# Kernel tuning notes

Measured on AMD Instinct MI355X. Metric: run time of the kernel, lower is better.

## Reference

```python
import jax, jax.numpy as jnp
import numpy as np

B, P, H, D = 32, 512, 512, 512

def setup_inputs() -> dict:
    key = jax.random.key(0)
    k1, k2, k3, k4 = jax.random.split(key, 4)
    px = jax.random.normal(k1, (B, P, D), dtype=jnp.float32)
    hx = jax.random.normal(k2, (B, H, D), dtype=jnp.float32)
    p_mask = jax.random.randint(k3, (B, P), 0, 2) == 1  # True = padded
    h_mask = jax.random.randint(k4, (B, H), 0, 2) == 1
    return {"px": px, "hx": hx, "p_mask": p_mask, "h_mask": h_mask}

def reference(px, hx, p_mask, h_mask):
    # shared (unscaled) score matrix: [B, P, H]
    e = jnp.einsum('bpd,bhd->bph', px, hx)
    neg_inf = jnp.float32(-jnp.inf)
    h_bias = jnp.where(h_mask, neg_inf, 0.0).astype(e.dtype)  # [B, H]
    p_bias = jnp.where(p_mask, neg_inf, 0.0).astype(e.dtype)  # [B, P]
    # softmax over hypothesis axis -> attend px to hx
    weight_b = jax.nn.softmax(e + h_bias[:, None, :], axis=2)  # [B, P, H]
    px_hat = jnp.einsum('bph,bhd->bpd', weight_b, hx)
    # softmax over premise axis -> attend hx to px
    weight_a = jax.nn.softmax(e + p_bias[:, :, None], axis=1)  # [B, P, H]
    hx_hat = jnp.einsum('bph,bpd->bhd', weight_a, px)
    m_p = jnp.concatenate([px, px_hat, px - px_hat, px * px_hat], axis=-1)
    m_h = jnp.concatenate([hx, hx_hat, hx - hx_hat, hx * hx_hat], axis=-1)
    return (m_p, m_h)
```

## Files before the change

kernel.cpp:

```cpp
#include <hip/hip_runtime.h>
#include <math.h>

#define NB 32
#define NN 512
#define ROWC 2048ull

typedef __attribute__((ext_vector_type(8))) short bf16x8;
typedef __attribute__((ext_vector_type(4))) float f32x4;

__device__ __forceinline__ unsigned int fbits(float f) {
  union { float f; unsigned int u; } v; v.f = f; return v.u;
}
__device__ __forceinline__ float bcast(unsigned int u) {
  union { unsigned int u; float f; } v; v.u = u; return v.f;
}
__device__ __forceinline__ unsigned int bf16_rne(float f) {
  unsigned int b = fbits(f);
  return (b + 0x7FFFu + ((b >> 16) & 1u)) >> 16;
}

__device__ __forceinline__ float wave_red_max(float v) {
#pragma unroll
  for (int o = 32; o > 0; o >>= 1) v = fmaxf(v, __shfl_down(v, o));
  return v;
}
__device__ __forceinline__ float wave_red_sum(float v) {
#pragma unroll
  for (int o = 32; o > 0; o >>= 1) v += __shfl_down(v, o);
  return v;
}

__device__ __forceinline__ int frag_byte(int blk, int lane, int khalf) {
  int base = ((((khalf << 3) + blk) << 6) + lane) << 4;
  int swz = (blk ^ (lane >> 4) ^ (khalf << 2)) & 7;
  return base ^ (swz << 4);
}

__device__ __forceinline__ void stage_hilo(const float* __restrict__ src, int row0, int k0,
                                           char* __restrict__ Lh, char* __restrict__ Ll,
                                           int t) {
#pragma unroll
  for (int i = 0; i < 8; ++i) {
    int idx = i * 256 + t;
    int r = idx >> 4, c4 = idx & 15;
    int k = c4 << 2;
    float4 f = *(const float4*)&src[(size_t)(row0 + r) * NN + k0 + k];
    unsigned int b0 = fbits(f.x), b1 = fbits(f.y), b2 = fbits(f.z), b3 = fbits(f.w);
    unsigned int h01 = (b0 >> 16) | (b1 & 0xFFFF0000u);
    unsigned int h23 = (b2 >> 16) | (b3 & 0xFFFF0000u);
    float r0 = f.x - bcast(b0 & 0xFFFF0000u);
    float r1 = f.y - bcast(b1 & 0xFFFF0000u);
    float r2 = f.z - bcast(b2 & 0xFFFF0000u);
    float r3 = f.w - bcast(b3 & 0xFFFF0000u);
    unsigned int l01 = (fbits(r0) >> 16) | (fbits(r1) & 0xFFFF0000u);
    unsigned int l23 = (fbits(r2) >> 16) | (fbits(r3) & 0xFFFF0000u);
    int khalf = k >> 5, k8 = (k >> 3) & 3, j = k & 7;
    int byte = frag_byte(r >> 4, (r & 15) + (k8 << 4), khalf) + (j << 1);
    *(uint2*)(Lh + byte) = make_uint2(h01, h23);
    *(uint2*)(Ll + byte) = make_uint2(l01, l23);
  }
}

__global__ __launch_bounds__(256) void gemm_e(const float* __restrict__ px,
                                              const float* __restrict__ hx,
                                              float* __restrict__ e) {
  __shared__ char Ah[16384], Al[16384], Bh[16384], Bl[16384];
  const int b = blockIdx.z;
  const float* A = px + (size_t)b * NN * NN;
  const float* B = hx + (size_t)b * NN * NN;
  float* C = e + (size_t)b * NN * NN;
  const int row0 = blockIdx.y * 128, col0 = blockIdx.x * 128;
  const int t = threadIdx.x;
  const int l = t & 63, w = t >> 6;
  const int wr = w >> 1, wc = w & 1;

  f32x4 acc[4][4];
#pragma unroll
  for (int i = 0; i < 4; ++i)
#pragma unroll
    for (int j = 0; j < 4; ++j)
#pragma unroll
      for (int r = 0; r < 4; ++r) acc[i][j][r] = 0.f;

  for (int k0 = 0; k0 < NN; k0 += 64) {
    stage_hilo(A, row0, k0, Ah, Al, t);
    stage_hilo(B, col0, k0, Bh, Bl, t);
    __syncthreads();
#pragma unroll
    for (int kh = 0; kh < 2; ++kh) {
      bf16x8 ah[4], al[4], bh[4], bl[4];
#pragma unroll
      for (int i = 0; i < 4; ++i) {
        int ab = frag_byte(wr * 4 + i, l, kh);
        ah[i] = *(const bf16x8*)(Ah + ab);
        al[i] = *(const bf16x8*)(Al + ab);
        int bb = frag_byte(wc * 4 + i, l, kh);
        bh[i] = *(const bf16x8*)(Bh + bb);
        bl[i] = *(const bf16x8*)(Bl + bb);
      }
#pragma unroll
      for (int i = 0; i < 4; ++i)
#pragma unroll
        for (int j = 0; j < 4; ++j) {
          acc[i][j] = __builtin_amdgcn_mfma_f32_16x16x32_bf16(ah[i], bh[j], acc[i][j], 0, 0, 0);
          acc[i][j] = __builtin_amdgcn_mfma_f32_16x16x32_bf16(ah[i], bl[j], acc[i][j], 0, 0, 0);
          acc[i][j] = __builtin_amdgcn_mfma_f32_16x16x32_bf16(al[i], bh[j], acc[i][j], 0, 0, 0);
        }
    }
    __syncthreads();
  }
  const int g = l >> 4, li = l & 15;
#pragma unroll
  for (int i = 0; i < 4; ++i)
#pragma unroll
    for (int j = 0; j < 4; ++j)
#pragma unroll
      for (int r = 0; r < 4; ++r) {
        int row = row0 + wr * 64 + i * 16 + g * 4 + r;
        int col = col0 + wc * 64 + j * 16 + li;
        C[(size_t)row * NN + col] = acc[i][j][r];
      }
}

__global__ __launch_bounds__(256) void softmax_h(const float* __restrict__ e,
                                                 const int* __restrict__ h_mask,
                                                 unsigned short* __restrict__ wb) {
  const int bp = blockIdx.x;
  const int b = bp >> 9;
  const float* row = e + (size_t)bp * NN;
  unsigned short* outp = wb + (size_t)bp * NN;
  const int* hm = h_mask + (size_t)b * NN;
  const int t = threadIdx.x;
  float2 v = *(const float2*)&row[2 * t];
  int2 m = *(const int2*)&hm[2 * t];
  float v0 = m.x ? -INFINITY : v.x;
  float v1 = m.y ? -INFINITY : v.y;
  __shared__ float pm[4], ps[4];
  float mx = wave_red_max(fmaxf(v0, v1));
  if ((t & 63) == 0) pm[t >> 6] = mx;
  __syncthreads();
  mx = fmaxf(fmaxf(pm[0], pm[1]), fmaxf(pm[2], pm[3]));
  float e0 = __expf(v0 - mx), e1 = __expf(v1 - mx);
  float s = wave_red_sum(e0 + e1);
  if ((t & 63) == 0) ps[t >> 6] = s;
  __syncthreads();
  s = ps[0] + ps[1] + ps[2] + ps[3];
  float inv = 1.0f / s;
  unsigned int u0 = bf16_rne(e0 * inv), u1 = bf16_rne(e1 * inv);
  *(unsigned int*)&outp[2 * t] = u0 | (u1 << 16);
}

__global__ __launch_bounds__(256) void softmax_p(const float* __restrict__ e,
                                                 const int* __restrict__ p_mask,
                                                 unsigned short* __restrict__ waT) {
  const int b = blockIdx.y;
  const int h0 = blockIdx.x * 32;
  const int t = threadIdx.x;
  const int tx = t & 31, ty = t >> 5;
  const float* eb = e + (size_t)b * NN * NN;
  const int* pmask = p_mask + (size_t)b * NN;
  const int h = h0 + tx;
  float val[64];
  float mx = -INFINITY;
#pragma unroll
  for (int k = 0; k < 64; ++k) {
    int p = ty + (k << 3);
    float v = pmask[p] ? -INFINITY : eb[(size_t)p * NN + h];
    val[k] = v;
    mx = fmaxf(mx, v);
  }
  __shared__ float rm[8][33];
  __shared__ unsigned short tile[32][516];
  rm[ty][tx] = mx;
  __syncthreads();
  float gm = rm[0][tx];
#pragma unroll
  for (int rr = 1; rr < 8; ++rr) gm = fmaxf(gm, rm[rr][tx]);
  float s = 0.f;
#pragma unroll
  for (int k = 0; k < 64; ++k) {
    val[k] = __expf(val[k] - gm);
    s += val[k];
  }
  __syncthreads();
  rm[ty][tx] = s;
  __syncthreads();
  float gs = rm[0][tx];
#pragma unroll
  for (int rr = 1; rr < 8; ++rr) gs += rm[rr][tx];
  float inv = 1.0f / gs;
#pragma unroll
  for (int k = 0; k < 64; ++k) {
    int p = ty + (k << 3);
    tile[tx][p] = (unsigned short)bf16_rne(val[k] * inv);
  }
  __syncthreads();
  unsigned short* wt = waT + ((size_t)b * NN + h0) * NN;
#pragma unroll
  for (int i = 0; i < 16; ++i) {
    int idx = i * 256 + t;
    int r = idx >> 7, c4 = idx & 127;
    *(uint2*)&wt[(size_t)r * NN + c4 * 4] = *(const uint2*)&tile[r][c4 * 4];
  }
}

__global__ __launch_bounds__(256) void gemm_wv(const unsigned short* __restrict__ Wg,
                                               const float* __restrict__ Bsrc,
                                               const float* __restrict__ Xg,
                                               float* __restrict__ outg) {
  __shared__ union {
    struct { char A[16384]; char B[16384]; } s;
    float ep[64][132];
  } u;
  const int b = blockIdx.z;
  const unsigned short* A = Wg + (size_t)b * NN * NN;
  const float* B = Bsrc + (size_t)b * NN * NN;
  const float* X = Xg + (size_t)b * NN * NN;
  float* out = outg + (size_t)b * NN * ROWC;
  const int row0 = blockIdx.y * 128, col0 = blockIdx.x * 128;
  const int t = threadIdx.x;
  const int l = t & 63, w = t >> 6;
  const int wr = w >> 1, wc = w & 1;

  f32x4 acc[4][4];
#pragma unroll
  for (int i = 0; i < 4; ++i)
#pragma unroll
    for (int j = 0; j < 4; ++j)
#pragma unroll
      for (int r = 0; r < 4; ++r) acc[i][j][r] = 0.f;

  for (int k0 = 0; k0 < NN; k0 += 64) {
#pragma unroll
    for (int i = 0; i < 8; ++i) {
      int idx = i * 256 + t;
      int r = idx >> 4, c4 = idx & 15, k = c4 << 2;
      uint2 v = *(const uint2*)&A[(size_t)(row0 + r) * NN + k0 + k];
      int khalf = k >> 5, k8 = (k >> 3) & 3, j = k & 7;
      int byte = frag_byte(r >> 4, (r & 15) + (k8 << 4), khalf) + (j << 1);
      *(uint2*)(u.s.A + byte) = v;
    }
#pragma unroll
    for (int i = 0; i < 4; ++i) {
      int idx = i * 256 + t;
      int kp = idx >> 5, nq = idx & 31;
      int k = kp << 1, n = nq << 2;
      const float* p0 = &B[(size_t)(k0 + k) * NN + col0 + n];
      float4 f0 = *(const float4*)p0;
      float4 f1 = *(const float4*)(p0 + NN);
      int khalf = k >> 5, k8 = (k >> 3) & 3, j = k & 7;
      float fa0[4] = {f0.x, f0.y, f0.z, f0.w};
      float fa1[4] = {f1.x, f1.y, f1.z, f1.w};
#pragma unroll
      for (int c = 0; c < 4; ++c) {
        unsigned int pk = bf16_rne(fa0[c]) | (bf16_rne(fa1[c]) << 16);
        int nn2 = n + c;
        int byte = frag_byte(nn2 >> 4, (nn2 & 15) + (k8 << 4), khalf) + (j << 1);
        *(unsigned int*)(u.s.B + byte) = pk;
      }
    }
    __syncthreads();
#pragma unroll
    for (int kh = 0; kh < 2; ++kh) {
      bf16x8 av[4], bv[4];
#pragma unroll
      for (int i = 0; i < 4; ++i) {
        av[i] = *(const bf16x8*)(u.s.A + frag_byte(wr * 4 + i, l, kh));
        bv[i] = *(const bf16x8*)(u.s.B + frag_byte(wc * 4 + i, l, kh));
      }
#pragma unroll
      for (int i = 0; i < 4; ++i)
#pragma unroll
        for (int j = 0; j < 4; ++j)
          acc[i][j] = __builtin_amdgcn_mfma_f32_16x16x32_bf16(av[i], bv[j], acc[i][j], 0, 0, 0);
    }
    __syncthreads();
  }

  const int g = l >> 4, li = l & 15;
#pragma unroll
  for (int pass = 0; pass < 2; ++pass) {
    if (wr == pass) {
#pragma unroll
      for (int i = 0; i < 4; ++i)
#pragma unroll
        for (int j = 0; j < 4; ++j)
#pragma unroll
          for (int r = 0; r < 4; ++r)
            u.ep[i * 16 + g * 4 + r][wc * 64 + j * 16 + li] = acc[i][j][r];
    }
    __syncthreads();
#pragma unroll
    for (int i = 0; i < 8; ++i) {
      int idx = i * 256 + t;
      int r = idx >> 5, c4 = idx & 31;
      int grow = row0 + pass * 64 + r;
      float4 ph = *(const float4*)&u.ep[r][c4 * 4];
      float4 xv = *(const float4*)&X[(size_t)grow * NN + col0 + c4 * 4];
      size_t base = (size_t)grow * ROWC + col0 + c4 * 4;
      *(float4*)&out[base] = xv;
      *(float4*)&out[base + 512] = ph;
      float4 df = {xv.x - ph.x, xv.y - ph.y, xv.z - ph.z, xv.w - ph.w};
      *(float4*)&out[base + 1024] = df;
      float4 pr = {xv.x * ph.x, xv.y * ph.y, xv.z * ph.z, xv.w * ph.w};
      *(float4*)&out[base + 1536] = pr;
    }
    __syncthreads();
  }
}

extern "C" void kernel_launch(void* const* d_in, const int* in_sizes, int n_in,
                              void* d_out, int out_size, void* d_ws, size_t ws_size,
                              hipStream_t stream) {
  const float* px = (const float*)d_in[0];
  const float* hx = (const float*)d_in[1];
  const int* p_mask = (const int*)d_in[2];
  const int* h_mask = (const int*)d_in[3];
  float* out = (float*)d_out;

  float* e = (float*)d_ws;
  unsigned short* wb = (unsigned short*)(e + (size_t)NB * NN * NN);
  unsigned short* waT = wb + (size_t)NB * NN * NN;

  dim3 blk(256);
  dim3 gg(4, 4, NB);
  gemm_e<<<gg, blk, 0, stream>>>(px, hx, e);
  softmax_h<<<dim3(NB * NN), blk, 0, stream>>>(e, h_mask, wb);
  softmax_p<<<dim3(16, NB), blk, 0, stream>>>(e, p_mask, waT);
  gemm_wv<<<gg, blk, 0, stream>>>(wb, hx, px, out);
  gemm_wv<<<gg, blk, 0, stream>>>(waT, px, hx, out + (size_t)NB * NN * ROWC);
}
```

Before: 242.6 us.

## Fuse softmax statistics into score GEMM epilogue and recompute weights in consumer GEMMs

Result: faster. 214.8 us (-11.5%).

```diff
diff --git a/kernel.cpp b/kernel.cpp
--- a/kernel.cpp
+++ b/kernel.cpp
@@ -17,17 +17,6 @@
 __device__ __forceinline__ unsigned int bf16_rne(float f) {
   unsigned int b = fbits(f);
   return (b + 0x7FFFu + ((b >> 16) & 1u)) >> 16;
-}
-
-__device__ __forceinline__ float wave_red_max(float v) {
-#pragma unroll
-  for (int o = 32; o > 0; o >>= 1) v = fmaxf(v, __shfl_down(v, o));
-  return v;
-}
-__device__ __forceinline__ float wave_red_sum(float v) {
-#pragma unroll
-  for (int o = 32; o > 0; o >>= 1) v += __shfl_down(v, o);
-  return v;
 }
 
 __device__ __forceinline__ int frag_byte(int blk, int lane, int khalf) {
@@ -61,10 +50,15 @@
   }
 }
 
-__global__ __launch_bounds__(256) void gemm_e(const float* __restrict__ px,
-                                              const float* __restrict__ hx,
-                                              float* __restrict__ e) {
+__global__ __launch_bounds__(256) void gemm_e_stats(
+    const float* __restrict__ px, const float* __restrict__ hx,
+    const int* __restrict__ p_mask, const int* __restrict__ h_mask,
+    float* __restrict__ e,
+    float* __restrict__ rpm, float* __restrict__ rps,
+    float* __restrict__ cpm, float* __restrict__ cps) {
   __shared__ char Ah[16384], Al[16384], Bh[16384], Bl[16384];
+  __shared__ int pmk[128], hmk[128];
+  __shared__ float st_m[2][128], st_s[2][128], sc_m[2][128], sc_s[2][128];
   const int b = blockIdx.z;
   const float* A = px + (size_t)b * NN * NN;
   const float* B = hx + (size_t)b * NN * NN;
@@ -73,6 +67,10 @@
   const int t = threadIdx.x;
   const int l = t & 63, w = t >> 6;
   const int wr = w >> 1, wc = w & 1;
+  const int g = l >> 4, li = l & 15;
+
+  if (t < 128) pmk[t] = p_mask[(size_t)b * NN + row0 + t];
+  else hmk[t - 128] = h_mask[(size_t)b * NN + col0 + (t - 128)];
 
   f32x4 acc[4][4];
 #pragma unroll
@@ -109,7 +107,7 @@
     }
     __syncthreads();
   }
-  const int g = l >> 4, li = l & 15;
+
 #pragma unroll
   for (int i = 0; i < 4; ++i)
 #pragma unroll
@@ -120,108 +118,132 @@
         int col = col0 + wc * 64 + j * 16 + li;
         C[(size_t)row * NN + col] = acc[i][j][r];
       }
-}
-
-__global__ __launch_bounds__(256) void softmax_h(const float* __restrict__ e,
-                                                 const int* __restrict__ h_mask,
-                                                 unsigned short* __restrict__ wb) {
-  const int bp = blockIdx.x;
-  const int b = bp >> 9;
-  const float* row = e + (size_t)bp * NN;
-  unsigned short* outp = wb + (size_t)bp * NN;
-  const int* hm = h_mask + (size_t)b * NN;
+
+#pragma unroll
+  for (int i = 0; i < 4; ++i)
+#pragma unroll
+    for (int r = 0; r < 4; ++r) {
+      float v[4];
+      float m = -INFINITY;
+#pragma unroll
+      for (int j = 0; j < 4; ++j) {
+        v[j] = hmk[wc * 64 + j * 16 + li] ? -INFINITY : acc[i][j][r];
+        m = fmaxf(m, v[j]);
+      }
+#pragma unroll
+      for (int o = 1; o < 16; o <<= 1) m = fmaxf(m, __shfl_xor(m, o));
+      float s = 0.f;
+#pragma unroll
+      for (int j = 0; j < 4; ++j) s += (v[j] == -INFINITY) ? 0.f : __expf(v[j] - m);
+#pragma unroll
+      for (int o = 1; o < 16; o <<= 1) s += __shfl_xor(s, o);
+      if (li == 0) {
+        st_m[wc][wr * 64 + i * 16 + g * 4 + r] = m;
+        st_s[wc][wr * 64 + i * 16 + g * 4 + r] = s;
+      }
+    }
+
+#pragma unroll
+  for (int j = 0; j < 4; ++j) {
+    float v[16];
+    float m = -INFINITY;
+#pragma unroll
+    for (int i = 0; i < 4; ++i)
+#pragma unroll
+      for (int r = 0; r < 4; ++r) {
+        float x = pmk[wr * 64 + i * 16 + g * 4 + r] ? -INFINITY : acc[i][j][r];
+        v[i * 4 + r] = x;
+        m = fmaxf(m, x);
+      }
+    m = fmaxf(m, __shfl_xor(m, 16));
+    m = fmaxf(m, __shfl_xor(m, 32));
+    float s = 0.f;
+#pragma unroll
+    for (int q = 0; q < 16; ++q) s += (v[q] == -INFINITY) ? 0.f : __expf(v[q] - m);
+    s += __shfl_xor(s, 16);
+    s += __shfl_xor(s, 32);
+    if (g == 0) {
+      sc_m[wr][wc * 64 + j * 16 + li] = m;
+      sc_s[wr][wc * 64 + j * 16 + li] = s;
+    }
+  }
+  __syncthreads();
+
+  if (t < 128) {
+    float m0 = st_m[0][t], m1 = st_m[1][t];
+    float s0 = st_s[0][t], s1 = st_s[1][t];
+    float m = fmaxf(m0, m1);
+    float s = 0.f;
+    if (s0 > 0.f) s += s0 * __expf(m0 - m);
+    if (s1 > 0.f) s += s1 * __expf(m1 - m);
+    rpm[((size_t)b * 4 + blockIdx.x) * NN + row0 + t] = m;
+    rps[((size_t)b * 4 + blockIdx.x) * NN + row0 + t] = s;
+  } else {
+    int c = t - 128;
+    float m0 = sc_m[0][c], m1 = sc_m[1][c];
+    float s0 = sc_s[0][c], s1 = sc_s[1][c];
+    float m = fmaxf(m0, m1);
+    float s = 0.f;
+    if (s0 > 0.f) s += s0 * __expf(m0 - m);
+    if (s1 > 0.f) s += s1 * __expf(m1 - m);
+    cpm[((size_t)b * 4 + blockIdx.y) * NN + col0 + c] = m;
+    cps[((size_t)b * 4 + blockIdx.y) * NN + col0 + c] = s;
+  }
+}
+
+__global__ __launch_bounds__(512) void merge_stats(
+    const float* __restrict__ rpm, const float* __restrict__ rps,
+    const float* __restrict__ cpm, const float* __restrict__ cps,
+    float* __restrict__ rmax, float* __restrict__ rinv,
+    float* __restrict__ cmax, float* __restrict__ cinv) {
+  const int b = blockIdx.x;
   const int t = threadIdx.x;
-  float2 v = *(const float2*)&row[2 * t];
-  int2 m = *(const int2*)&hm[2 * t];
-  float v0 = m.x ? -INFINITY : v.x;
-  float v1 = m.y ? -INFINITY : v.y;
-  __shared__ float pm[4], ps[4];
-  float mx = wave_red_max(fmaxf(v0, v1));
-  if ((t & 63) == 0) pm[t >> 6] = mx;
-  __syncthreads();
-  mx = fmaxf(fmaxf(pm[0], pm[1]), fmaxf(pm[2], pm[3]));
-  float e0 = __expf(v0 - mx), e1 = __expf(v1 - mx);
-  float s = wave_red_sum(e0 + e1);
-  if ((t & 63) == 0) ps[t >> 6] = s;
-  __syncthreads();
-  s = ps[0] + ps[1] + ps[2] + ps[3];
-  float inv = 1.0f / s;
-  unsigned int u0 = bf16_rne(e0 * inv), u1 = bf16_rne(e1 * inv);
-  *(unsigned int*)&outp[2 * t] = u0 | (u1 << 16);
-}
-
-__global__ __launch_bounds__(256) void softmax_p(const float* __restrict__ e,
-                                                 const int* __restrict__ p_mask,
-                                                 unsigned short* __restrict__ waT) {
-  const int b = blockIdx.y;
-  const int h0 = blockIdx.x * 32;
-  const int t = threadIdx.x;
-  const int tx = t & 31, ty = t >> 5;
-  const float* eb = e + (size_t)b * NN * NN;
-  const int* pmask = p_mask + (size_t)b * NN;
-  const int h = h0 + tx;
-  float val[64];
-  float mx = -INFINITY;
-#pragma unroll
-  for (int k = 0; k < 64; ++k) {
-    int p = ty + (k << 3);
-    float v = pmask[p] ? -INFINITY : eb[(size_t)p * NN + h];
-    val[k] = v;
-    mx = fmaxf(mx, v);
-  }
-  __shared__ float rm[8][33];
-  __shared__ unsigned short tile[32][516];
-  rm[ty][tx] = mx;
-  __syncthreads();
-  float gm = rm[0][tx];
-#pragma unroll
-  for (int rr = 1; rr < 8; ++rr) gm = fmaxf(gm, rm[rr][tx]);
+  const float* pm = blockIdx.y == 0 ? rpm : cpm;
+  const float* ps = blockIdx.y == 0 ? rps : cps;
+  float* fm = blockIdx.y == 0 ? rmax : cmax;
+  float* fi = blockIdx.y == 0 ? rinv : cinv;
+  float mj[4], sj[4];
+  float m = -INFINITY;
+#pragma unroll
+  for (int j = 0; j < 4; ++j) {
+    mj[j] = pm[((size_t)b * 4 + j) * NN + t];
+    sj[j] = ps[((size_t)b * 4 + j) * NN + t];
+    m = fmaxf(m, mj[j]);
+  }
   float s = 0.f;
 #pragma unroll
-  for (int k = 0; k < 64; ++k) {
-    val[k] = __expf(val[k] - gm);
-    s += val[k];
-  }
-  __syncthreads();
-  rm[ty][tx] = s;
-  __syncthreads();
-  float gs = rm[0][tx];
-#pragma unroll
-  for (int rr = 1; rr < 8; ++rr) gs += rm[rr][tx];
-  float inv = 1.0f / gs;
-#pragma unroll
-  for (int k = 0; k < 64; ++k) {
-    int p = ty + (k << 3);
-    tile[tx][p] = (unsigned short)bf16_rne(val[k] * inv);
-  }
-  __syncthreads();
-  unsigned short* wt = waT + ((size_t)b * NN + h0) * NN;
-#pragma unroll
-  for (int i = 0; i < 16; ++i) {
-    int idx = i * 256 + t;
-    int r = idx >> 7, c4 = idx & 127;
-    *(uint2*)&wt[(size_t)r * NN + c4 * 4] = *(const uint2*)&tile[r][c4 * 4];
-  }
-}
-
-__global__ __launch_bounds__(256) void gemm_wv(const unsigned short* __restrict__ Wg,
-                                               const float* __restrict__ Bsrc,
-                                               const float* __restrict__ Xg,
-                                               float* __restrict__ outg) {
+  for (int j = 0; j < 4; ++j)
+    if (sj[j] > 0.f) s += sj[j] * __expf(mj[j] - m);
+  fm[(size_t)b * NN + t] = m;
+  fi[(size_t)b * NN + t] = 1.0f / s;
+}
+
+__global__ __launch_bounds__(256) void gemm_wp(
+    const float* __restrict__ E, const float* __restrict__ hxg,
+    const float* __restrict__ pxg, const int* __restrict__ h_mask,
+    const float* __restrict__ rmax, const float* __restrict__ rinv,
+    float* __restrict__ outg) {
   __shared__ union {
     struct { char A[16384]; char B[16384]; } s;
     float ep[64][132];
   } u;
   const int b = blockIdx.z;
-  const unsigned short* A = Wg + (size_t)b * NN * NN;
-  const float* B = Bsrc + (size_t)b * NN * NN;
-  const float* X = Xg + (size_t)b * NN * NN;
+  const float* Eb = E + (size_t)b * NN * NN;
+  const float* B = hxg + (size_t)b * NN * NN;
+  const float* X = pxg + (size_t)b * NN * NN;
+  const int* hm = h_mask + (size_t)b * NN;
+  const float* rmx = rmax + (size_t)b * NN;
+  const float* rin = rinv + (size_t)b * NN;
   float* out = outg + (size_t)b * NN * ROWC;
   const int row0 = blockIdx.y * 128, col0 = blockIdx.x * 128;
   const int t = threadIdx.x;
   const int l = t & 63, w = t >> 6;
   const int wr = w >> 1, wc = w & 1;
 
+  float rmv[8];
+#pragma unroll
+  for (int i = 0; i < 8; ++i) rmv[i] = rmx[row0 + ((i * 256 + t) >> 4)];
+
   f32x4 acc[4][4];
 #pragma unroll
   for (int i = 0; i < 4; ++i)
@@ -235,10 +257,17 @@
     for (int i = 0; i < 8; ++i) {
       int idx = i * 256 + t;
       int r = idx >> 4, c4 = idx & 15, k = c4 << 2;
-      uint2 v = *(const uint2*)&A[(size_t)(row0 + r) * NN + k0 + k];
+      float4 f = *(const float4*)&Eb[(size_t)(row0 + r) * NN + k0 + k];
+      int4 m4 = *(const int4*)&hm[k0 + k];
+      float w0 = m4.x ? 0.f : __expf(f.x - rmv[i]);
+      float w1 = m4.y ? 0.f : __expf(f.y - rmv[i]);
+      float w2 = m4.z ? 0.f : __expf(f.z - rmv[i]);
+      float w3 = m4.w ? 0.f : __expf(f.w - rmv[i]);
+      unsigned int p01 = bf16_rne(w0) | (bf16_rne(w1) << 16);
+      unsigned int p23 = bf16_rne(w2) | (bf16_rne(w3) << 16);
       int khalf = k >> 5, k8 = (k >> 3) & 3, j = k & 7;
       int byte = frag_byte(r >> 4, (r & 15) + (k8 << 4), khalf) + (j << 1);
-      *(uint2*)(u.s.A + byte) = v;
+      *(uint2*)(u.s.A + byte) = make_uint2(p01, p23);
     }
 #pragma unroll
     for (int i = 0; i < 4; ++i) {
@@ -295,7 +324,9 @@
       int idx = i * 256 + t;
       int r = idx >> 5, c4 = idx & 31;
       int grow = row0 + pass * 64 + r;
+      float ri = rin[grow];
       float4 ph = *(const float4*)&u.ep[r][c4 * 4];
+      ph.x *= ri; ph.y *= ri; ph.z *= ri; ph.w *= ri;
       float4 xv = *(const float4*)&X[(size_t)grow * NN + col0 + c4 * 4];
       size_t base = (size_t)grow * ROWC + col0 + c4 * 4;
       *(float4*)&out[base] = xv;
@@ -309,6 +340,139 @@
   }
 }
 
+__global__ __launch_bounds__(256) void gemm_wh(
+    const float* __restrict__ E, const float* __restrict__ pxg,
+    const float* __restrict__ hxg, const int* __restrict__ p_mask,
+    const float* __restrict__ cmax, const float* __restrict__ cinv,
+    float* __restrict__ outg) {
+  __shared__ union {
+    struct { char A[16384]; char B[16384]; } s;
+    float ep[64][132];
+  } u;
+  const int b = blockIdx.z;
+  const float* Eb = E + (size_t)b * NN * NN;
+  const float* B = pxg + (size_t)b * NN * NN;
+  const float* X = hxg + (size_t)b * NN * NN;
+  const int* pmsk = p_mask + (size_t)b * NN;
+  const float* cmx = cmax + (size_t)b * NN;
+  const float* cin = cinv + (size_t)b * NN;
+  float* out = outg + (size_t)b * NN * ROWC;
+  const int row0 = blockIdx.y * 128, col0 = blockIdx.x * 128;
+  const int t = threadIdx.x;
+  const int l = t & 63, w = t >> 6;
+  const int wr = w >> 1, wc = w & 1;
+
+  float4 cmv[4];
+#pragma unroll
+  for (int i = 0; i < 4; ++i) {
+    int idx = i * 256 + t;
+    int n = (idx & 31) << 2;
+    cmv[i] = *(const float4*)&cmx[row0 + n];
+  }
+
+  f32x4 acc[4][4];
+#pragma unroll
+  for (int i = 0; i < 4; ++i)
+#pragma unroll
+    for (int j = 0; j < 4; ++j)
+#pragma unroll
+      for (int r = 0; r < 4; ++r) acc[i][j][r] = 0.f;
+
+  for (int k0 = 0; k0 < NN; k0 += 64) {
+#pragma unroll
+    for (int i = 0; i < 4; ++i) {
+      int idx = i * 256 + t;
+      int kp = idx >> 5, nq = idx & 31;
+      int k = kp << 1, n = nq << 2;
+      const float* p0 = &Eb[(size_t)(k0 + k) * NN + row0 + n];
+      float4 f0 = *(const float4*)p0;
+      float4 f1 = *(const float4*)(p0 + NN);
+      int pm0 = pmsk[k0 + k], pm1 = pmsk[k0 + k + 1];
+      float fa0[4] = {f0.x, f0.y, f0.z, f0.w};
+      float fa1[4] = {f1.x, f1.y, f1.z, f1.w};
+      float cma[4] = {cmv[i].x, cmv[i].y, cmv[i].z, cmv[i].w};
+      int khalf = k >> 5, k8 = (k >> 3) & 3, j = k & 7;
+#pragma unroll
+      for (int c = 0; c < 4; ++c) {
+        float w0 = pm0 ? 0.f : __expf(fa0[c] - cma[c]);
+        float w1 = pm1 ? 0.f : __expf(fa1[c] - cma[c]);
+        unsigned int pk = bf16_rne(w0) | (bf16_rne(w1) << 16);
+        int nn2 = n + c;
+        int byte = frag_byte(nn2 >> 4, (nn2 & 15) + (k8 << 4), khalf) + (j << 1);
+        *(unsigned int*)(u.s.A + byte) = pk;
+      }
+    }
+#pragma unroll
+    for (int i = 0; i < 4; ++i) {
+      int idx = i * 256 + t;
+      int kp = idx >> 5, nq = idx & 31;
+      int k = kp << 1, n = nq << 2;
+      const float* p0 = &B[(size_t)(k0 + k) * NN + col0 + n];
+      float4 f0 = *(const float4*)p0;
+      float4 f1 = *(const float4*)(p0 + NN);
+      int khalf = k >> 5, k8 = (k >> 3) & 3, j = k & 7;
+      float fa0[4] = {f0.x, f0.y, f0.z, f0.w};
+      float fa1[4] = {f1.x, f1.y, f1.z, f1.w};
+#pragma unroll
+      for (int c = 0; c < 4; ++c) {
+        unsigned int pk = bf16_rne(fa0[c]) | (bf16_rne(fa1[c]) << 16);
+        int nn2 = n + c;
+        int byte = frag_byte(nn2 >> 4, (nn2 & 15) + (k8 << 4), khalf) + (j << 1);
+        *(unsigned int*)(u.s.B + byte) = pk;
+      }
+    }
+    __syncthreads();
+#pragma unroll
+    for (int kh = 0; kh < 2; ++kh) {
+      bf16x8 av[4], bv[4];
+#pragma unroll
+      for (int i = 0; i < 4; ++i) {
+        av[i] = *(const bf16x8*)(u.s.A + frag_byte(wr * 4 + i, l, kh));
+        bv[i] = *(const bf16x8*)(u.s.B + frag_byte(wc * 4 + i, l, kh));
+      }
+#pragma unroll
+      for (int i = 0; i < 4; ++i)
+#pragma unroll
+        for (int j = 0; j < 4; ++j)
+          acc[i][j] = __builtin_amdgcn_mfma_f32_16x16x32_bf16(av[i], bv[j], acc[i][j], 0, 0, 0);
+    }
+    __syncthreads();
+  }
+
+  const int g = l >> 4, li = l & 15;
+#pragma unroll
+  for (int pass = 0; pass < 2; ++pass) {
+    if (wr == pass) {
+#pragma unroll
+      for (int i = 0; i < 4; ++i)
+#pragma unroll
+        for (int j = 0; j < 4; ++j)
+#pragma unroll
+          for (int r = 0; r < 4; ++r)
+            u.ep[i * 16 + g * 4 + r][wc * 64 + j * 16 + li] = acc[i][j][r];
+    }
+    __syncthreads();
+#pragma unroll
+    for (int i = 0; i < 8; ++i) {
+      int idx = i * 256 + t;
+      int r = idx >> 5, c4 = idx & 31;
+      int grow = row0 + pass * 64 + r;
+      float ci = cin[grow];
+      float4 hh = *(const float4*)&u.ep[r][c4 * 4];
+      hh.x *= ci; hh.y *= ci; hh.z *= ci; hh.w *= ci;
+      float4 xv = *(const float4*)&X[(size_t)grow * NN + col0 + c4 * 4];
+      size_t base = (size_t)grow * ROWC + col0 + c4 * 4;
+      *(float4*)&out[base] = xv;
+      *(float4*)&out[base + 512] = hh;
+      float4 df = {xv.x - hh.x, xv.y - hh.y, xv.z - hh.z, xv.w - hh.w};
+      *(float4*)&out[base + 1024] = df;
+      float4 pr = {xv.x * hh.x, xv.y * hh.y, xv.z * hh.z, xv.w * hh.w};
+      *(float4*)&out[base + 1536] = pr;
+    }
+    __syncthreads();
+  }
+}
+
 extern "C" void kernel_launch(void* const* d_in, const int* in_sizes, int n_in,
                               void* d_out, int out_size, void* d_ws, size_t ws_size,
                               hipStream_t stream) {
@@ -318,15 +482,22 @@
   const int* h_mask = (const int*)d_in[3];
   float* out = (float*)d_out;
 
-  float* e = (float*)d_ws;
-  unsigned short* wb = (unsigned short*)(e + (size_t)NB * NN * NN);
-  unsigned short* waT = wb + (size_t)NB * NN * NN;
+  float* E = (float*)d_ws;
+  float* rpm = E + (size_t)NB * NN * NN;
+  float* rps = rpm + (size_t)NB * 4 * NN;
+  float* cpm = rps + (size_t)NB * 4 * NN;
+  float* cps = cpm + (size_t)NB * 4 * NN;
+  float* rmaxv = cps + (size_t)NB * 4 * NN;
+  float* rinvv = rmaxv + (size_t)NB * NN;
+  float* cmaxv = rinvv + (size_t)NB * NN;
+  float* cinvv = cmaxv + (size_t)NB * NN;
 
   dim3 blk(256);
   dim3 gg(4, 4, NB);
-  gemm_e<<<gg, blk, 0, stream>>>(px, hx, e);
-  softmax_h<<<dim3(NB * NN), blk, 0, stream>>>(e, h_mask, wb);
-  softmax_p<<<dim3(16, NB), blk, 0, stream>>>(e, p_mask, waT);
-  gemm_wv<<<gg, blk, 0, stream>>>(wb, hx, px, out);
-  gemm_wv<<<gg, blk, 0, stream>>>(waT, px, hx, out + (size_t)NB * NN * ROWC);
-}
+  gemm_e_stats<<<gg, blk, 0, stream>>>(px, hx, p_mask, h_mask, E, rpm, rps, cpm, cps);
+  merge_stats<<<dim3(NB, 2), dim3(512), 0, stream>>>(rpm, rps, cpm, cps,
+                                                     rmaxv, rinvv, cmaxv, cinvv);
+  gemm_wp<<<gg, blk, 0, stream>>>(E, hx, px, h_mask, rmaxv, rinvv, out);
+  gemm_wh<<<gg, blk, 0, stream>>>(E, px, hx, p_mask, cmaxv, cinvv,
+                                  out + (size_t)NB * NN * ROWC);
+}
```
